# Optimization experiments

Hardware: AMD Instinct MI355X
Metric: run time of the kernel (lower is better)

## Reference

```python
import jax, jax.numpy as jnp
import numpy as np
from jax import lax

NH = 8        # num_heads
C = 256       # embedding_dim
WS = 5        # window_size
DN = ('NCHW', 'OIHW', 'NCHW')


def setup_inputs() -> dict:
    key = jax.random.key(0)
    ks = jax.random.split(key, 6)
    B, H, W = 16, 64, 64
    hd = C // NH  # per-head dim = pos_embed_dim
    return {
        "src": jax.random.normal(ks[0], (B, C, H, W), jnp.float32),
        "rel_pos_embed": jax.random.normal(ks[1], (hd, WS, WS), jnp.float32) * 0.02,
        "qkv_w": jax.random.normal(ks[2], (3 * C, C), jnp.float32) * (C ** -0.5),
        "cpe_w": jax.random.normal(ks[3], (C, C, 3, 3), jnp.float32) * (1.0 / np.sqrt(C * 9)),
        "cpe_b": jnp.zeros((C,), jnp.float32),
        "out_w": jax.random.normal(ks[4], (C, C), jnp.float32) * (C ** -0.5),
        "out_b": jnp.zeros((C,), jnp.float32),
    }


def reference(src, rel_pos_embed, qkv_w, cpe_w, cpe_b, out_w, out_b):
    B, Cc, H, W = src.shape
    hd = Cc // NH
    scale = hd ** -0.5

    # conv positional encoding (3x3 conv) + residual
    x = lax.conv_general_dilated(src, cpe_w, (1, 1), [(1, 1), (1, 1)],
                                 dimension_numbers=DN) + cpe_b[None, :, None, None] + src

    # 1x1 qkv conv as a GEMM over channels
    qkv = jnp.einsum('oc,bchw->bohw', qkv_w, x)
    q, k, v = jnp.split(qkv, 3, axis=1)
    q = q.reshape(B * NH, hd, H, W)
    k = k.reshape(B * NH, hd, H, W)
    v = v.reshape(B * NH, hd, H, W)

    # linear (lambda) attention: softmax over spatial positions of k
    kf = jax.nn.softmax(k.reshape(B * NH, hd, H * W), axis=-1)   # (b' i n)
    vf = v.reshape(B * NH, hd, H * W)                            # (b' o n)
    content_lambda = jnp.einsum('bin,bon->bio', kf, vf)          # (b' i o), tiny
    qf = q.reshape(B * NH, hd, H * W) * scale
    content = jnp.einsum('bin,bio->bon', qf, content_lambda).reshape(B * NH, hd, H, W)

    # depthwise conv positional lambda on v
    pad = WS // 2
    pos_lambda = lax.conv_general_dilated(v, rel_pos_embed[:, None], (1, 1),
                                          [(pad, pad), (pad, pad)],
                                          dimension_numbers=DN,
                                          feature_group_count=hd)
    result = (content + q * pos_lambda).reshape(B, Cc, H, W)

    # 1x1 output projection
    return jnp.einsum('oc,bchw->bohw', out_w, result) + out_b[None, :, None, None]
```

## Files before the change

### kernel.cpp

```cpp
#include <hip/hip_runtime.h>


typedef unsigned short u16;
typedef __bf16 bf16x8 __attribute__((ext_vector_type(8)));
typedef float f32x4 __attribute__((ext_vector_type(4)));
#define HW 4096

__device__ __forceinline__ float bf2f(u16 u){
  unsigned v = ((unsigned)u) << 16;
  return __builtin_bit_cast(float, v);
}
__device__ __forceinline__ u16 f2bf(float f){
  unsigned u = __builtin_bit_cast(unsigned, f);
  u = u + 0x7fffu + ((u >> 16) & 1u);
  return (u16)(u >> 16);
}
__device__ __forceinline__ unsigned pack2(float a, float b){
  return (unsigned)f2bf(a) | ((unsigned)f2bf(b) << 16);
}
__device__ __forceinline__ void unpack2(unsigned u, float& a, float& b){
  a = bf2f((u16)(u & 0xffffu)); b = bf2f((u16)(u >> 16));
}
__device__ __forceinline__ void unp8(uint4 r, float* v){
  unpack2(r.x, v[0], v[1]); unpack2(r.y, v[2], v[3]);
  unpack2(r.z, v[4], v[5]); unpack2(r.w, v[6], v[7]);
}

__device__ __forceinline__ void gl2lds16(const u16* g, u16* l){
  __builtin_amdgcn_global_load_lds((__attribute__((address_space(1))) void*)g,
                                   (__attribute__((address_space(3))) void*)l, 16, 0, 0);
}

__global__ void zero_border(u16* __restrict__ xpad){
  int idx = blockIdx.x*256 + threadIdx.x;
  int g = idx & 31;
  int p = idx >> 5;
  int b = p / 260; int r = p - b*260;
  int y, x;
  if (r < 66)      { y = 0;      x = r; }
  else if (r < 132){ y = 65;     x = r-66; }
  else if (r < 196){ y = r-131;  x = 0; }
  else             { y = r-195;  x = 65; }
  *(uint4*)&xpad[((size_t)b*4356 + (size_t)y*66 + x)*256 + g*8] = uint4{0,0,0,0};
}

__global__ __launch_bounds__(256) void to_nhwc(const float* __restrict__ src,
                                               u16* __restrict__ xpad){
  __shared__ u16 sl[64*264];
  const int t = threadIdx.x, w = t>>6, lane = t&63;
  const int y = blockIdx.x, b = blockIdx.y;
  for (int cc = 0; cc < 64; ++cc){
    const int c = cc*4 + w;
    float v = src[((size_t)(b*256 + c))*HW + y*64 + lane];
    sl[lane*264 + c] = f2bf(v);
  }
  __syncthreads();
  #pragma unroll
  for (int i = 0; i < 8; ++i){
    int idx = t + 256*i;
    int p = idx >> 5, g = idx & 31;
    uint4 v = *(const uint4*)&sl[p*264 + g*8];
    *(uint4*)&xpad[((size_t)b*4356 + (size_t)(y+1)*66 + (p+1))*256 + g*8] = v;
  }
}

__global__ void repack_w(const float* __restrict__ cpe_w, const float* __restrict__ qkv_w,
                         const float* __restrict__ out_w, u16* __restrict__ wrb,
                         u16* __restrict__ wq, u16* __restrict__ wo){
  int idx = blockIdx.x*256 + threadIdx.x;
  if (idx < 589824){
    int kk = idx >> 16, o = (idx >> 8) & 255, c = idx & 255;
    wrb[idx] = f2bf(cpe_w[((o*256 + c)*9) + kk]);
  } else if (idx < 786432){
    int j = idx - 589824;
    wq[j] = f2bf(qkv_w[j]);
  } else {
    int j = idx - 786432;
    wo[j] = f2bf(out_w[j]);
  }
}

__global__ __launch_bounds__(512, 2) void conv_mfma(const u16* __restrict__ xpad,
    const u16* __restrict__ wrb, const float* __restrict__ bias,
    u16* __restrict__ xout){
  __shared__ u16 As[32768];
  __shared__ u16 Bs[32768];
  const int t = threadIdx.x, w8 = t>>6, lane = t&63;
  const int idx = blockIdx.x;
  const int nb = (idx&7)*32 + (idx>>3);
  const int pg = nb*256;
  const int b = pg>>12, row0 = (pg&4095)>>6;
  const size_t xb = (size_t)b*4356;
  const int dstb = w8*2048 + lane*8;
  const u16* aP[4]; const u16* bP[4];
  #pragma unroll
  for (int i = 0; i < 4; ++i){
    int G = (w8*4+i)*64 + lane;
    int p = G>>3, gs = (G&7) ^ (p&7);
    aP[i] = xpad + (xb + (size_t)(row0 + (p>>6) + 1)*66 + (p&63) + 1)*256 + gs*8;
    bP[i] = wrb + (size_t)p*256 + gs*8;
  }
  const int wm = w8>>2, wn = w8&3;
  const int qd = lane>>4;
  int a_off[8], b_off[4];
  #pragma unroll
  for (int m = 0; m < 8; ++m){
    int p = wm*128 + m*16 + (lane&15);
    a_off[m] = p*64 + ((qd ^ (p&7)) << 3);
  }
  #pragma unroll
  for (int n = 0; n < 4; ++n){
    int r = wn*64 + n*16 + (lane&15);
    b_off[n] = r*64 + ((qd ^ (r&7)) << 3);
  }
  f32x4 acc[8][4];
  #pragma unroll
  for (int i=0;i<8;++i)
    #pragma unroll
    for (int j=0;j<4;++j) acc[i][j] = f32x4{0.f,0.f,0.f,0.f};

  auto STAGE = [&](const int bufo, const int s){
    int c9 = s/9, tap = s - c9*9, ky = tap/3, kx = tap - ky*3;
    int offA = ((ky-1)*66 + (kx-1))*256 + c9*64;
    int offB = tap*65536 + c9*64;
    #pragma unroll
    for (int i = 0; i < 4; ++i){
      gl2lds16(aP[i] + offA, &As[bufo + dstb + i*512]);
      gl2lds16(bP[i] + offB, &Bs[bufo + dstb + i*512]);
    }
  };
  auto COMPUTE = [&](const int bufo){
    __builtin_amdgcn_s_setprio(1);
    #pragma unroll
    for (int kh = 0; kh < 2; ++kh){
      bf16x8 af[8], bfr[4];
      #pragma unroll
      for (int m = 0; m < 8; ++m)
        af[m] = __builtin_bit_cast(bf16x8, *(const uint4*)&As[bufo + (a_off[m] ^ (kh<<5))]);
      #pragma unroll
      for (int n = 0; n < 4; ++n)
        bfr[n] = __builtin_bit_cast(bf16x8, *(const uint4*)&Bs[bufo + (b_off[n] ^ (kh<<5))]);
      #pragma unroll
      for (int mt = 0; mt < 8; ++mt)
        #pragma unroll
        for (int nt = 0; nt < 4; ++nt)
          acc[mt][nt] = __builtin_amdgcn_mfma_f32_16x16x32_bf16(bfr[nt], af[mt], acc[mt][nt], 0,0,0);
    }
    __builtin_amdgcn_s_setprio(0);
  };
  #define SYNC asm volatile("s_waitcnt vmcnt(0)" ::: "memory"); __builtin_amdgcn_s_barrier();

  STAGE(0, 0);
  SYNC
  for (int s2 = 0; s2 < 18; ++s2){
    STAGE(16384, 2*s2+1);
    COMPUTE(0);
    SYNC
    if (s2 < 17) STAGE(0, 2*s2+2);
    COMPUTE(16384);
    SYNC
  }
  #pragma unroll
  for (int nt = 0; nt < 4; ++nt){
    const int och4 = wn*64 + nt*16 + qd*4;
    float4 b4 = *(const float4*)&bias[och4];
    #pragma unroll
    for (int mt = 0; mt < 8; ++mt){
      const int px = wm*128 + mt*16 + (lane&15);
      const int y = row0 + (px>>6), x = px&63;
      ushort4 r4 = *(const ushort4*)&xpad[(xb + (size_t)(y+1)*66 + x + 1)*256 + och4];
      ushort4 s;
      s.x = f2bf(acc[mt][nt][0] + b4.x + bf2f(r4.x));
      s.y = f2bf(acc[mt][nt][1] + b4.y + bf2f(r4.y));
      s.z = f2bf(acc[mt][nt][2] + b4.z + bf2f(r4.z));
      s.w = f2bf(acc[mt][nt][3] + b4.w + bf2f(r4.w));
      *(ushort4*)&xout[(size_t)(pg + px)*256 + och4] = s;
    }
  }
  #undef SYNC
}

template<int NO, int NOT>
__global__ __launch_bounds__(512, 2) void gemm_mfma(const u16* __restrict__ act,
    const u16* __restrict__ wt, void* __restrict__ out){
  __shared__ u16 As[32768];
  __shared__ u16 Bs[32768];
  const int t = threadIdx.x, w8 = t>>6, lane = t&63;
  const int idx = blockIdx.x;
  const int x8 = idx&7, q = idx>>3;
  const int ot = q % NOT, nb = x8*32 + q / NOT;
  const int pg = nb*256, o0 = ot*256;
  const int dstb = w8*2048 + lane*8;
  const u16* aP[4]; const u16* bP[4];
  #pragma unroll
  for (int i = 0; i < 4; ++i){
    int G = (w8*4+i)*64 + lane;
    int p = G>>3, gs = (G&7) ^ (p&7);
    aP[i] = act + (size_t)(pg + p)*256 + gs*8;
    bP[i] = wt  + (size_t)(o0 + p)*256 + gs*8;
  }
  const int wm = w8>>2, wn = w8&3;
  const int qd = lane>>4;
  int a_off[8], b_off[4];
  #pragma unroll
  for (int m = 0; m < 8; ++m){
    int p = wm*128 + m*16 + (lane&15);
    a_off[m] = p*64 + ((qd ^ (p&7)) << 3);
  }
  #pragma unroll
  for (int n = 0; n < 4; ++n){
    int r = wn*64 + n*16 + (lane&15);
    b_off[n] = r*64 + ((qd ^ (r&7)) << 3);
  }
  f32x4 acc[8][4];
  #pragma unroll
  for (int i=0;i<8;++i)
    #pragma unroll
    for (int j=0;j<4;++j) acc[i][j] = f32x4{0.f,0.f,0.f,0.f};

  auto STAGE = [&](const int bufo, const int s){
    const int c0 = s*64;
    #pragma unroll
    for (int i = 0; i < 4; ++i){
      gl2lds16(aP[i] + c0, &As[bufo + dstb + i*512]);
      gl2lds16(bP[i] + c0, &Bs[bufo + dstb + i*512]);
    }
  };
  auto COMPUTE = [&](const int bufo){
    __builtin_amdgcn_s_setprio(1);
    #pragma unroll
    for (int kh = 0; kh < 2; ++kh){
      bf16x8 af[8], bfr[4];
      #pragma unroll
      for (int m = 0; m < 8; ++m)
        af[m] = __builtin_bit_cast(bf16x8, *(const uint4*)&As[bufo + (a_off[m] ^ (kh<<5))]);
      #pragma unroll
      for (int n = 0; n < 4; ++n)
        bfr[n] = __builtin_bit_cast(bf16x8, *(const uint4*)&Bs[bufo + (b_off[n] ^ (kh<<5))]);
      #pragma unroll
      for (int mt = 0; mt < 8; ++mt)
        #pragma unroll
        for (int nt = 0; nt < 4; ++nt)
          acc[mt][nt] = __builtin_amdgcn_mfma_f32_16x16x32_bf16(bfr[nt], af[mt], acc[mt][nt], 0,0,0);
    }
    __builtin_amdgcn_s_setprio(0);
  };
  #define SYNC asm volatile("s_waitcnt vmcnt(0)" ::: "memory"); __builtin_amdgcn_s_barrier();

  STAGE(0, 0);
  SYNC
  for (int s2 = 0; s2 < 2; ++s2){
    STAGE(16384, 2*s2+1);
    COMPUTE(0);
    SYNC
    if (s2 < 1) STAGE(0, 2*s2+2);
    COMPUTE(16384);
    SYNC
  }
  u16* op = (u16*)out;
  #pragma unroll
  for (int nt = 0; nt < 4; ++nt){
    const int och4 = o0 + wn*64 + nt*16 + qd*4;
    #pragma unroll
    for (int mt = 0; mt < 8; ++mt){
      const int px = wm*128 + mt*16 + (lane&15);
      ushort4 s;
      s.x = f2bf(acc[mt][nt][0]); s.y = f2bf(acc[mt][nt][1]);
      s.z = f2bf(acc[mt][nt][2]); s.w = f2bf(acc[mt][nt][3]);
      *(ushort4*)&op[(size_t)(pg + px)*NO + och4] = s;
    }
  }
  #undef SYNC
}

__global__ __launch_bounds__(512, 2) void gemm_out(const u16* __restrict__ qkv,
    const u16* __restrict__ qpos, const u16* __restrict__ Mb,
    const u16* __restrict__ wo, const float* __restrict__ bias,
    float* __restrict__ out){
  __shared__ u16 As[32768];
  __shared__ u16 Bs[32768];
  const int t = threadIdx.x, w8 = t>>6, lane = t&63;
  const int idx = blockIdx.x;
  const int nb = (idx&7)*32 + (idx>>3);
  const int pg = nb*256;
  const int b = pg>>12, hw0 = pg&4095;
  const int dstb = w8*2048 + lane*8;
  const u16 *aQ[4], *aX[4], *bM[4], *bW[4];
  #pragma unroll
  for (int i = 0; i < 4; ++i){
    int G = (w8*4+i)*64 + lane;
    int p = G>>3, gs = (G&7) ^ (p&7);
    aQ[i] = qkv  + (size_t)(pg + p)*768 + gs*8;
    aX[i] = qpos + (size_t)(pg + p)*256 + gs*8;
    bM[i] = Mb   + ((size_t)b*256 + p)*256 + gs*8;
    bW[i] = wo   + (size_t)p*256 + gs*8;
  }
  const int wm = w8>>2, wn = w8&3;
  const int qd = lane>>4;
  int a_off[8], b_off[4];
  #pragma unroll
  for (int m = 0; m < 8; ++m){
    int p = wm*128 + m*16 + (lane&15);
    a_off[m] = p*64 + ((qd ^ (p&7)) << 3);
  }
  #pragma unroll
  for (int n = 0; n < 4; ++n){
    int r = wn*64 + n*16 + (lane&15);
    b_off[n] = r*64 + ((qd ^ (r&7)) << 3);
  }
  f32x4 acc[8][4];
  #pragma unroll
  for (int i=0;i<8;++i)
    #pragma unroll
    for (int j=0;j<4;++j) acc[i][j] = f32x4{0.f,0.f,0.f,0.f};

  auto STAGE = [&](const int bufo, const int s){
    #pragma unroll
    for (int i = 0; i < 4; ++i){
      const u16* sa = (s < 4) ? (aQ[i] + s*64)      : (aX[i] + (s-4)*64);
      const u16* sb = (s < 4) ? (bM[i] + s*64)      : (bW[i] + (s-4)*64);
      gl2lds16(sa, &As[bufo + dstb + i*512]);
      gl2lds16(sb, &Bs[bufo + dstb + i*512]);
    }
  };
  auto COMPUTE = [&](const int bufo){
    __builtin_amdgcn_s_setprio(1);
    #pragma unroll
    for (int kh = 0; kh < 2; ++kh){
      bf16x8 af[8], bfr[4];
      #pragma unroll
      for (int m = 0; m < 8; ++m)
        af[m] = __builtin_bit_cast(bf16x8, *(const uint4*)&As[bufo + (a_off[m] ^ (kh<<5))]);
      #pragma unroll
      for (int n = 0; n < 4; ++n)
        bfr[n] = __builtin_bit_cast(bf16x8, *(const uint4*)&Bs[bufo + (b_off[n] ^ (kh<<5))]);
      #pragma unroll
      for (int mt = 0; mt < 8; ++mt)
        #pragma unroll
        for (int nt = 0; nt < 4; ++nt)
          acc[mt][nt] = __builtin_amdgcn_mfma_f32_16x16x32_bf16(af[mt], bfr[nt], acc[mt][nt], 0,0,0);
    }
    __builtin_amdgcn_s_setprio(0);
  };
  #define SYNC asm volatile("s_waitcnt vmcnt(0)" ::: "memory"); __builtin_amdgcn_s_barrier();

  STAGE(0, 0);
  SYNC
  #pragma unroll
  for (int s2 = 0; s2 < 4; ++s2){
    STAGE(16384, 2*s2+1);
    COMPUTE(0);
    SYNC
    if (s2 < 3) STAGE(0, 2*s2+2);
    COMPUTE(16384);
    SYNC
  }
  const int col = lane&15, row_l = qd*4;
  #pragma unroll
  for (int nt = 0; nt < 4; ++nt){
    const int och = wn*64 + nt*16 + col;
    const float bo2 = bias[och];
    #pragma unroll
    for (int mt = 0; mt < 8; ++mt){
      const int pl = wm*128 + mt*16 + row_l;
      float4 v;
      v.x = acc[mt][nt][0]+bo2; v.y = acc[mt][nt][1]+bo2;
      v.z = acc[mt][nt][2]+bo2; v.w = acc[mt][nt][3]+bo2;
      *(float4*)&out[((size_t)b*256 + och)*HW + hw0 + pl] = v;
    }
  }
  #undef SYNC
}

__global__ void zero_cl(float* __restrict__ cl){
  cl[blockIdx.x*256 + threadIdx.x] = 0.f;
}

__global__ __launch_bounds__(64) void lambda_kern(const u16* __restrict__ qkv,
                                                  float* __restrict__ cl,
                                                  float* __restrict__ S){
  __shared__ float Kl[64*36];
  __shared__ float Vl[64*36];
  const int t = threadIdx.x;
  const int bp = blockIdx.x, split = blockIdx.y;
  const int b = bp>>3, h = bp&7;
  const int ig = t&7, og = t>>3;
  float acc[4][4];
  float sacc[4] = {0.f,0.f,0.f,0.f};
  #pragma unroll
  for (int i=0;i<4;++i)
    #pragma unroll
    for (int j=0;j<4;++j) acc[i][j] = 0.f;
  for (int chunk = 0; chunk < 8; ++chunk){
    const int n = split*512 + chunk*64 + t;
    const u16* kp = qkv + (size_t)(b*HW + n)*768 + 256 + h*32;
    const u16* vp = kp + 256;
    uint4 k4[4], v4[4];
    #pragma unroll
    for (int qq=0;qq<4;++qq){ k4[qq] = ((const uint4*)kp)[qq]; v4[qq] = ((const uint4*)vp)[qq]; }
    __syncthreads();
    #pragma unroll
    for (int qq=0;qq<4;++qq){
      float kv[8], vv[8]; unp8(k4[qq], kv); unp8(v4[qq], vv);
      #pragma unroll
      for (int e=0;e<8;++e) kv[e] = __expf(kv[e]);
      *(float4*)&Kl[t*36 + qq*8]     = float4{kv[0],kv[1],kv[2],kv[3]};
      *(float4*)&Kl[t*36 + qq*8 + 4] = float4{kv[4],kv[5],kv[6],kv[7]};
      *(float4*)&Vl[t*36 + qq*8]     = float4{vv[0],vv[1],vv[2],vv[3]};
      *(float4*)&Vl[t*36 + qq*8 + 4] = float4{vv[4],vv[5],vv[6],vv[7]};
    }
    __syncthreads();
    for (int p = 0; p < 64; ++p){
      float4 kf = *(const float4*)&Kl[p*36 + ig*4];
      float4 vf = *(const float4*)&Vl[p*36 + og*4];
      float kfa[4] = {kf.x,kf.y,kf.z,kf.w};
      float vfa[4] = {vf.x,vf.y,vf.z,vf.w};
      #pragma unroll
      for (int i=0;i<4;++i){
        sacc[i] += kfa[i];
        #pragma unroll
        for (int j=0;j<4;++j) acc[i][j] = fmaf(kfa[i], vfa[j], acc[i][j]);
      }
    }
  }
  #pragma unroll
  for (int i=0;i<4;++i)
    #pragma unroll
    for (int j=0;j<4;++j)
      atomicAdd(&cl[(size_t)bp*1024 + (ig*4+i)*32 + og*4+j], acc[i][j]);
  if (og == 0){
    #pragma unroll
    for (int i=0;i<4;++i) atomicAdd(&S[bp*32 + ig*4 + i], sacc[i]);
  }
}

__global__ __launch_bounds__(256) void mb_kern(const float* __restrict__ cl,
    const float* __restrict__ S, const float* __restrict__ out_w,
    u16* __restrict__ Mb){
  __shared__ float clS[1024];
  __shared__ float sinv[32];
  const int t = threadIdx.x;
  const int h = blockIdx.x & 7, b = blockIdx.x >> 3;
  const int bp = b*8 + h;
  for (int idx = t; idx < 1024; idx += 256)
    clS[idx] = cl[(size_t)bp*1024 + idx];
  if (t < 32) sinv[t] = 0.17677669529663687f / S[bp*32 + t];
  __syncthreads();
  float wrow[32];
  #pragma unroll
  for (int o = 0; o < 32; ++o) wrow[o] = out_w[t*256 + h*32 + o];
  u16 out16[32];
  #pragma unroll
  for (int i = 0; i < 32; ++i){
    float a = 0.f;
    #pragma unroll
    for (int o = 0; o < 32; ++o) a = fmaf(wrow[o], clS[i*32+o], a);
    out16[i] = f2bf(a * sinv[i]);
  }
  u16* mp = Mb + ((size_t)b*256 + t)*256 + h*32;
  #pragma unroll
  for (int g = 0; g < 4; ++g)
    ((uint4*)mp)[g] = *(uint4*)&out16[g*8];
}

__global__ __launch_bounds__(256) void pos_combine(const u16* __restrict__ qkv,
    const float* __restrict__ rel, u16* __restrict__ res){
  __shared__ u16 vt[12800];
  __shared__ float relT[800];
  const int t = threadIdx.x;
  const int tile = blockIdx.x, h = blockIdx.y, b = blockIdx.z;
  const int x0 = (tile&3)*16, y0 = (tile>>2)*16;
  for (int idx = t; idx < 800; idx += 256){
    int tap = idx>>5, ch = idx&31;
    relT[idx] = rel[ch*25 + tap];
  }
  #pragma unroll
  for (int i = 0; i < 7; ++i){
    int idx = t + 256*i;
    if (idx < 1600){
      int hp = idx>>2, g = idx&3;
      int hy = hp/20, hx = hp - hy*20;
      int y = y0 + hy - 2, x = x0 + hx - 2;
      uint4 v = uint4{0,0,0,0};
      if ((unsigned)y < 64u && (unsigned)x < 64u)
        v = *(const uint4*)&qkv[(size_t)(b*HW + y*64 + x)*768 + 512 + h*32 + g*8];
      *(uint4*)&vt[(g*400 + hp)*8] = v;
    }
  }
  __syncthreads();
  const int py = t>>4, px = t&15;
  const int pix = b*HW + (y0+py)*64 + x0 + px;
  const u16* qp = qkv + (size_t)pix*768 + h*32;
  float qv[32];
  {
    uint4 q0 = ((const uint4*)qp)[0], q1 = ((const uint4*)qp)[1];
    uint4 q2 = ((const uint4*)qp)[2], q3 = ((const uint4*)qp)[3];
    unp8(q0, qv); unp8(q1, qv+8); unp8(q2, qv+16); unp8(q3, qv+24);
  }
  float outv[32];
  #pragma unroll
  for (int chg = 0; chg < 4; ++chg){
    float pos[8];
    #pragma unroll
    for (int j=0;j<8;++j) pos[j] = 0.f;
    #pragma unroll
    for (int dy = 0; dy < 5; ++dy)
      #pragma unroll
      for (int dx = 0; dx < 5; ++dx){
        int hp = (py+dy)*20 + px + dx;
        uint4 v4 = *(const uint4*)&vt[(chg*400 + hp)*8];
        float vv[8]; unp8(v4, vv);
        float4 r0 = *(const float4*)&relT[(dy*5+dx)*32 + chg*8];
        float4 r1 = *(const float4*)&relT[(dy*5+dx)*32 + chg*8 + 4];
        pos[0]=fmaf(r0.x, vv[0], pos[0]); pos[1]=fmaf(r0.y, vv[1], pos[1]);
        pos[2]=fmaf(r0.z, vv[2], pos[2]); pos[3]=fmaf(r0.w, vv[3], pos[3]);
        pos[4]=fmaf(r1.x, vv[4], pos[4]); pos[5]=fmaf(r1.y, vv[5], pos[5]);
        pos[6]=fmaf(r1.z, vv[6], pos[6]); pos[7]=fmaf(r1.w, vv[7], pos[7]);
      }
    #pragma unroll
    for (int j=0;j<8;++j) outv[chg*8+j] = qv[chg*8+j] * pos[j];
  }
  u16* rp = res + (size_t)pix*256 + h*32;
  #pragma unroll
  for (int g = 0; g < 4; ++g){
    uint4 o_;
    o_.x = pack2(outv[g*8+0], outv[g*8+1]);
    o_.y = pack2(outv[g*8+2], outv[g*8+3]);
    o_.z = pack2(outv[g*8+4], outv[g*8+5]);
    o_.w = pack2(outv[g*8+6], outv[g*8+7]);
    ((uint4*)rp)[g] = o_;
  }
}

extern "C" void kernel_launch(void* const* d_in, const int* in_sizes, int n_in,
                              void* d_out, int out_size, void* d_ws, size_t ws_size,
                              hipStream_t stream) {
  const float* src   = (const float*)d_in[0];
  const float* rel   = (const float*)d_in[1];
  const float* qkv_w = (const float*)d_in[2];
  const float* cpe_w = (const float*)d_in[3];
  const float* cpe_b = (const float*)d_in[4];
  const float* out_w = (const float*)d_in[5];
  const float* out_b = (const float*)d_in[6];
  char* ws = (char*)d_ws;
  u16*   qkv  = (u16*)(ws);
  u16*   xpad = (u16*)(ws);
  u16*   xbuf = (u16*)(ws + 100663296);
  float* cl   = (float*)(ws + 134217728);
  float* S    = (float*)(ws + 134742016);
  u16*   wrb  = (u16*)(ws + 134758400);
  u16*   wq   = (u16*)(ws + 135938048);
  u16*   Mb   = (u16*)(ws + 134758400);
  u16*   wo   = (u16*)(ws + 136855552);

  zero_border<<<dim3(520), dim3(256), 0, stream>>>(xpad);
  to_nhwc<<<dim3(64, 16), dim3(256), 0, stream>>>(src, xpad);
  repack_w<<<dim3(3328), dim3(256), 0, stream>>>(cpe_w, qkv_w, out_w, wrb, wq, wo);
  conv_mfma<<<dim3(256), dim3(512), 0, stream>>>(xpad, wrb, cpe_b, xbuf);
  gemm_mfma<768,3><<<dim3(768), dim3(512), 0, stream>>>(xbuf, wq, (void*)qkv);
  zero_cl<<<dim3(528), dim3(256), 0, stream>>>(cl);
  lambda_kern<<<dim3(128, 8), dim3(64), 0, stream>>>(qkv, cl, S);
  mb_kern<<<dim3(128), dim3(256), 0, stream>>>(cl, S, out_w, Mb);
  pos_combine<<<dim3(16, 8, 16), dim3(256), 0, stream>>>(qkv, rel, xbuf);
  gemm_out<<<dim3(256), dim3(512), 0, stream>>>(qkv, xbuf, Mb, wo, out_b, (float*)d_out);
}
```

Before: 413.7 us.

## Reuse halo activation tile across all nine conv taps in LDS

```diff
diff --git a/kernel.cpp b/kernel.cpp
--- a/kernel.cpp
+++ b/kernel.cpp
@@ -83,7 +83,7 @@
 __global__ __launch_bounds__(512, 2) void conv_mfma(const u16* __restrict__ xpad,
     const u16* __restrict__ wrb, const float* __restrict__ bias,
     u16* __restrict__ xout){
-  __shared__ u16 As[32768];
+  __shared__ u16 Ah[25344];
   __shared__ u16 Bs[32768];
   const int t = threadIdx.x, w8 = t>>6, lane = t&63;
   const int idx = blockIdx.x;
@@ -91,22 +91,30 @@
   const int pg = nb*256;
   const int b = pg>>12, row0 = (pg&4095)>>6;
   const size_t xb = (size_t)b*4356;
-  const int dstb = w8*2048 + lane*8;
-  const u16* aP[4]; const u16* bP[4];
+  const u16* aHp[6]; const u16* aHt; const u16* bPn[4];
+  #pragma unroll
+  for (int i = 0; i < 6; ++i){
+    int G = i*512 + t, hp = G>>3, gs = (G&7) ^ (hp&7);
+    int hr = hp/66, hx = hp - hr*66;
+    aHp[i] = xpad + (xb + (size_t)(row0+hr)*66 + hx)*256 + gs*8;
+  }
+  {
+    int G = 3072 + t, hp = G>>3, gs = (G&7) ^ (hp&7);
+    int hr = hp/66, hx = hp - hr*66;
+    aHt = xpad + (xb + (size_t)(row0+hr)*66 + hx)*256 + gs*8;
+  }
   #pragma unroll
   for (int i = 0; i < 4; ++i){
-    int G = (w8*4+i)*64 + lane;
-    int p = G>>3, gs = (G&7) ^ (p&7);
-    aP[i] = xpad + (xb + (size_t)(row0 + (p>>6) + 1)*66 + (p&63) + 1)*256 + gs*8;
-    bP[i] = wrb + (size_t)p*256 + gs*8;
+    int G = i*512 + t, o = G>>3, gs = (G&7) ^ (o&7);
+    bPn[i] = wrb + (size_t)o*256 + gs*8;
   }
   const int wm = w8>>2, wn = w8&3;
   const int qd = lane>>4;
-  int a_off[8], b_off[4];
+  int hbase[8], b_off[4];
   #pragma unroll
   for (int m = 0; m < 8; ++m){
     int p = wm*128 + m*16 + (lane&15);
-    a_off[m] = p*64 + ((qd ^ (p&7)) << 3);
+    hbase[m] = (p>>6)*66 + (p&63);
   }
   #pragma unroll
   for (int n = 0; n < 4; ++n){
@@ -119,24 +127,33 @@
     #pragma unroll
     for (int j=0;j<4;++j) acc[i][j] = f32x4{0.f,0.f,0.f,0.f};
 
-  auto STAGE = [&](const int bufo, const int s){
-    int c9 = s/9, tap = s - c9*9, ky = tap/3, kx = tap - ky*3;
-    int offA = ((ky-1)*66 + (kx-1))*256 + c9*64;
-    int offB = tap*65536 + c9*64;
-    #pragma unroll
-    for (int i = 0; i < 4; ++i){
-      gl2lds16(aP[i] + offA, &As[bufo + dstb + i*512]);
-      gl2lds16(bP[i] + offB, &Bs[bufo + dstb + i*512]);
-    }
-  };
-  auto COMPUTE = [&](const int bufo){
+  auto STAGE_A = [&](const int c9o){
+    #pragma unroll
+    for (int i = 0; i < 6; ++i)
+      gl2lds16(aHp[i] + c9o, &Ah[(i*512 + t)*8]);
+    if (t < 96) gl2lds16(aHt + c9o, &Ah[(3072 + t)*8]);
+  };
+  auto STAGE_B = [&](const int bufo, const int s){
+    const int c9 = s/9, tap = s - c9*9;
+    const int soff = tap*65536 + c9*64;
+    #pragma unroll
+    for (int i = 0; i < 4; ++i)
+      gl2lds16(bPn[i] + soff, &Bs[bufo + (i*512 + t)*8]);
+  };
+  auto COMPUTE = [&](const int kyx, const int bufo){
     __builtin_amdgcn_s_setprio(1);
+    int aoff[8];
+    #pragma unroll
+    for (int m = 0; m < 8; ++m){
+      int hp = hbase[m] + kyx;
+      aoff[m] = hp*64 + ((qd ^ (hp&7)) << 3);
+    }
     #pragma unroll
     for (int kh = 0; kh < 2; ++kh){
       bf16x8 af[8], bfr[4];
       #pragma unroll
       for (int m = 0; m < 8; ++m)
-        af[m] = __builtin_bit_cast(bf16x8, *(const uint4*)&As[bufo + (a_off[m] ^ (kh<<5))]);
+        af[m] = __builtin_bit_cast(bf16x8, *(const uint4*)&Ah[aoff[m] ^ (kh<<5)]);
       #pragma unroll
       for (int n = 0; n < 4; ++n)
         bfr[n] = __builtin_bit_cast(bf16x8, *(const uint4*)&Bs[bufo + (b_off[n] ^ (kh<<5))]);
@@ -148,17 +165,23 @@
     }
     __builtin_amdgcn_s_setprio(0);
   };
-  #define SYNC asm volatile("s_waitcnt vmcnt(0)" ::: "memory"); __builtin_amdgcn_s_barrier();
-
-  STAGE(0, 0);
-  SYNC
-  for (int s2 = 0; s2 < 18; ++s2){
-    STAGE(16384, 2*s2+1);
-    COMPUTE(0);
-    SYNC
-    if (s2 < 17) STAGE(0, 2*s2+2);
-    COMPUTE(16384);
-    SYNC
+
+  STAGE_A(0);
+  STAGE_B(0, 0);
+  STAGE_B(16384, 1);
+  asm volatile("s_waitcnt vmcnt(4)" ::: "memory");
+  __builtin_amdgcn_s_barrier();
+  for (int s = 0; s < 36; ++s){
+    const int c9 = s/9, tap = s - c9*9;
+    const int kyx = (tap/3)*66 + (tap - (tap/3)*3);
+    COMPUTE(kyx, (s&1)*16384);
+    if (s == 35) break;
+    asm volatile("s_barrier" ::: "memory");
+    if (tap == 8) STAGE_A((c9+1)*64);
+    if (s <= 33) STAGE_B((s&1)*16384, s+2);
+    if (s == 34) { asm volatile("s_waitcnt vmcnt(0)" ::: "memory"); }
+    else         { asm volatile("s_waitcnt vmcnt(4)" ::: "memory"); }
+    __builtin_amdgcn_s_barrier();
   }
   #pragma unroll
   for (int nt = 0; nt < 4; ++nt){
@@ -177,7 +200,6 @@
       *(ushort4*)&xout[(size_t)(pg + px)*256 + och4] = s;
     }
   }
-  #undef SYNC
 }
 
 template<int NO, int NOT>
```

New measurement: 412.9 us. No clear change (-0.2%).
